# Optimization experiments

Measured on AMD Instinct MI355X. Metric: run time of the kernel, lower is better.

Reference implementation:

```python
import jax, jax.numpy as jnp
import numpy as np

_GELU = lambda x: jax.nn.gelu(x, approximate=False)  # torch nn.GELU default = exact erf


def setup_inputs():
    key = jax.random.key(0)
    ks = jax.random.split(key, 32)
    B, H = 16384, 768
    def p(i, shape):
        return jax.random.normal(ks[i], shape, jnp.float32) * 0.02
    return {
        "image_feat": jax.random.normal(ks[0], (B, H), jnp.float32),
        "text_feat": jax.random.normal(ks[1], (B, H), jnp.float32),
        "enhanced_image_feat": jax.random.normal(ks[2], (B, H), jnp.float32),
        "enhanced_text_feat": jax.random.normal(ks[3], (B, H), jnp.float32),
        "missing_type": jax.random.randint(ks[4], (B,), 0, 4),
        # info_encoder: H->256->64
        "info_w1": p(5, (H, 256)), "info_b1": jnp.zeros((256,), jnp.float32),
        "info_w2": p(6, (256, 64)), "info_b2": jnp.zeros((64,), jnp.float32),
        # modality_importance_predictor: H->H/2->1 (dropout inactive at eval)
        "imp_w1": p(7, (H, H // 2)), "imp_b1": jnp.zeros((H // 2,), jnp.float32),
        "imp_w2": p(8, (H // 2, 1)), "imp_b2": jnp.zeros((1,), jnp.float32),
        # feature_discriminator: H->256->64->1
        "disc_w1": p(9, (H, 256)), "disc_b1": jnp.zeros((256,), jnp.float32),
        "disc_w2": p(10, (256, 64)), "disc_b2": jnp.zeros((64,), jnp.float32),
        "disc_w3": p(11, (64, 1)), "disc_b3": jnp.zeros((1,), jnp.float32),
        # consistency_predictor: 2H->H->H/2->1
        "cons_w1": p(12, (2 * H, H)), "cons_b1": jnp.zeros((H,), jnp.float32),
        "cons_w2": p(13, (H, H // 2)), "cons_b2": jnp.zeros((H // 2,), jnp.float32),
        "cons_w3": p(14, (H // 2, 1)), "cons_b3": jnp.zeros((1,), jnp.float32),
        # task_difficulty_predictor: 2H->H->H/2->1
        "diff_w1": p(15, (2 * H, H)), "diff_b1": jnp.zeros((H,), jnp.float32),
        "diff_w2": p(16, (H, H // 2)), "diff_b2": jnp.zeros((H // 2,), jnp.float32),
        "diff_w3": p(17, (H // 2, 1)), "diff_b3": jnp.zeros((1,), jnp.float32),
    }


def _forward(image_feat, text_feat, enhanced_image_feat, enhanced_text_feat,
             info_w1, info_b1, info_w2, info_b2,
             imp_w1, imp_b1, imp_w2, imp_b2,
             disc_w1, disc_b1, disc_w2, disc_b2, disc_w3, disc_b3,
             cons_w1, cons_b1, cons_w2, cons_b2, cons_w3, cons_b3,
             diff_w1, diff_b1, diff_w2, diff_b2, diff_w3, diff_b3):
    sig = jax.nn.sigmoid

    def geometric(f):  # vectorized version of the per-sample python loop
        n = jnp.linalg.norm(f, axis=-1)
        nq = sig((n - 1.0) * 2.0)
        sp = jnp.mean((jnp.abs(f) > 0.01).astype(jnp.float32), axis=-1)
        sq = sig(jnp.std(f, axis=-1, ddof=1) * 10.0 - 1.0)  # torch.std is unbiased
        return (nq + sp + sq) / 3.0

    def information(f):
        enc = _GELU(f @ info_w1 + info_b1) @ info_w2 + info_b2  # [B,64]
        disc = jnp.round(sig(enc) * 10.0).astype(jnp.int32)     # values in 0..10
        # histogram-based entropy == the torch.unique loop (prob = count/64)
        counts = jnp.sum(disc[:, :, None] == jnp.arange(11, dtype=jnp.int32)[None, None, :], axis=1)
        prob = counts.astype(jnp.float32) / enc.shape[-1]
        ent = -jnp.sum(jnp.where(prob > 0, prob * jnp.log(prob + 1e-8), 0.0), axis=-1)
        eq = sig(ent - 2.0)
        # svd of a 1xD matrix has a single singular value = ||f||_2
        n = jnp.linalg.norm(f, axis=-1)
        cq = (n > 0.01).astype(jnp.float32) / f.shape[-1]
        fn = f / jnp.maximum(n, 1e-12)[:, None]  # F.normalize
        dq = sig(jnp.sum(fn * fn, axis=-1) - 0.5)
        return (eq + cq + dq) / 3.0

    def importance(f):
        return sig(_GELU(f @ imp_w1 + imp_b1) @ imp_w2 + imp_b2)[:, 0]

    def discrim(f):
        h = _GELU(f @ disc_w1 + disc_b1)
        h = _GELU(h @ disc_w2 + disc_b2)
        return sig(h @ disc_w3 + disc_b3)[:, 0]

    def head3(f, w1, b1, w2, b2, w3, b3):
        h = _GELU(f @ w1 + b1)
        h = _GELU(h @ w2 + b2)
        return sig(h @ w3 + b3)[:, 0]

    g_img = geometric(image_feat)
    g_txt = geometric(text_feat)
    g_eimg = geometric(enhanced_image_feat)
    g_etxt = geometric(enhanced_text_feat)
    i_img = information(image_feat)
    i_txt = information(text_feat)
    cons_o = head3(jnp.concatenate([image_feat, text_feat], -1), cons_w1, cons_b1, cons_w2, cons_b2, cons_w3, cons_b3)
    cons_e = head3(jnp.concatenate([enhanced_image_feat, enhanced_text_feat], -1), cons_w1, cons_b1, cons_w2, cons_b2, cons_w3, cons_b3)
    imp_i = importance(image_feat)
    imp_t = importance(text_feat)
    imp_ei = importance(enhanced_image_feat)
    imp_et = importance(enhanced_text_feat)
    auth_io = discrim(image_feat)
    auth_ie = discrim(enhanced_image_feat)
    auth_to = discrim(text_feat)
    auth_te = discrim(enhanced_text_feat)
    diff = head3(jnp.concatenate([enhanced_image_feat, enhanced_text_feat], -1), diff_w1, diff_b1, diff_w2, diff_b2, diff_w3, diff_b3)
    overall = (g_img + g_txt + i_img + i_txt + cons_e + (imp_i + imp_t) / 2.0) / 6.0
    return jnp.stack([g_img, g_txt, g_eimg, g_etxt, i_img, i_txt, cons_o, cons_e,
                      imp_i, imp_t, imp_ei, imp_et, auth_io, auth_ie, auth_to, auth_te,
                      diff, overall])  # [18, B]


def reference(image_feat, text_feat, enhanced_image_feat, enhanced_text_feat, missing_type,
              info_w1, info_b1, info_w2, info_b2,
              imp_w1, imp_b1, imp_w2, imp_b2,
              disc_w1, disc_b1, disc_w2, disc_b2, disc_w3, disc_b3,
              cons_w1, cons_b1, cons_w2, cons_b2, cons_w3, cons_b3,
              diff_w1, diff_b1, diff_w2, diff_b2, diff_w3, diff_b3):
    # missing_type is carried by the original forward but never used in the math
    return _forward(image_feat, text_feat, enhanced_image_feat, enhanced_text_feat,
                    info_w1, info_b1, info_w2, info_b2,
                    imp_w1, imp_b1, imp_w2, imp_b2,
                    disc_w1, disc_b1, disc_w2, disc_b2, disc_w3, disc_b3,
                    cons_w1, cons_b1, cons_w2, cons_b2, cons_w3, cons_b3,
                    diff_w1, diff_b1, diff_w2, diff_b2, diff_w3, diff_b3)
```

## Files before the change

### kernel.cpp

```cpp
#include <hip/hip_runtime.h>

typedef unsigned short bfu;
typedef __attribute__((ext_vector_type(8))) __bf16 bf16x8;
typedef __attribute__((ext_vector_type(4))) float f32x4;

__device__ __forceinline__ float bf2f(bfu u) {
    unsigned int x = ((unsigned int)u) << 16;
    return __builtin_bit_cast(float, x);
}
__device__ __forceinline__ bfu f2bf(float f) {
    unsigned int u = __builtin_bit_cast(unsigned int, f);
    unsigned int r = (u + 0x7fffu + ((u >> 16) & 1u)) >> 16;
    return (bfu)r;
}
__device__ __forceinline__ float sigm(float x) { return 1.0f / (1.0f + __expf(-x)); }
__device__ __forceinline__ float gelu_f(float x) {
    const float y = 0.7978845608f * (x + 0.044715f * x * x * x);
    const float t = 1.f - 2.f / (__expf(2.f * y) + 1.f);
    return 0.5f * x * (1.f + t);
}
__device__ __forceinline__ float gelu_x(float x) {
    return 0.5f * x * (1.0f + erff(x * 0.70710678118654752f));
}

__device__ __forceinline__ void async16(const void* g, void* l) {
    __builtin_amdgcn_global_load_lds((const __attribute__((address_space(1))) void*)g,
                                     (__attribute__((address_space(3))) void*)l, 16, 0, 0);
}

struct TDesc { const float* src; bfu* dst; int K, N, blk0; };
struct TPack { TDesc d[9]; };

__global__ __launch_bounds__(256) void transpose_k(TPack p) {
    const int bid = blockIdx.x;
    int j = 0;
#pragma unroll
    for (int i = 1; i < 9; ++i)
        if (bid >= p.d[i].blk0) j = i;
    const TDesc d = p.d[j];
    const int local = bid - d.blk0;
    const int tkn = d.K >> 6;
    const int tk = local % tkn, tn = local / tkn;
    const int k0 = tk * 64, n0 = tn * 64;
    __shared__ float tile[64][65];
    const int tx = threadIdx.x & 63, ty = threadIdx.x >> 6;
#pragma unroll
    for (int i = 0; i < 16; ++i) {
        const int r = ty * 16 + i;
        tile[r][tx] = d.src[(size_t)(k0 + r) * d.N + n0 + tx];
    }
    __syncthreads();
#pragma unroll
    for (int i = 0; i < 16; ++i) {
        const int n = ty * 16 + i;
        d.dst[(size_t)(n0 + n) * d.K + k0 + tx] = f2bf(tile[tx][n]);
    }
}

__global__ __launch_bounds__(256)
void prep_k(float* accz, int nacc, bfu* disc2pad, const float* w3,
            const float* b2, float* w3pad, float* b2pad) {
    const int i = blockIdx.x * 256 + threadIdx.x;
    if (i < nacc) accz[i] = 0.f;
    if (i < 64 * 256) disc2pad[64 * 256 + i] = 0;
    if (i < 128) {
        w3pad[i] = (i < 64) ? w3[i] : 0.f;
        b2pad[i] = (i < 64) ? b2[i] : 0.f;
    }
}

__global__ __launch_bounds__(256)
void geomcast_k(const float* F0, const float* F1, bfu* D0, bfu* D1,
                float* g0, float* g1, float* p0, float* p1) {
    const int z = blockIdx.y;
    const float* F = z ? F1 : F0;
    bfu* D = z ? D1 : D0;
    float* gout = z ? g1 : g0;
    float* part = z ? p1 : p0;
    const int wave = threadIdx.x >> 6, lane = threadIdx.x & 63;
    const int row = blockIdx.x * 4 + wave;
    const float* fr = F + (size_t)row * 768;
    bfu* dr = D + (size_t)row * 768;
    float sum = 0.f, ss = 0.f, cnt = 0.f;
#pragma unroll
    for (int i = 0; i < 3; ++i) {
        const float4 v = *(const float4*)(fr + i * 256 + lane * 4);
        sum += v.x + v.y + v.z + v.w;
        ss += v.x * v.x + v.y * v.y + v.z * v.z + v.w * v.w;
        cnt += ((fabsf(v.x) > 0.01f) ? 1.f : 0.f) + ((fabsf(v.y) > 0.01f) ? 1.f : 0.f) +
               ((fabsf(v.z) > 0.01f) ? 1.f : 0.f) + ((fabsf(v.w) > 0.01f) ? 1.f : 0.f);
        ushort4 b;
        b.x = f2bf(v.x); b.y = f2bf(v.y); b.z = f2bf(v.z); b.w = f2bf(v.w);
        *(ushort4*)(dr + i * 256 + lane * 4) = b;
    }
#pragma unroll
    for (int off = 32; off; off >>= 1) {
        sum += __shfl_xor(sum, off);
        ss  += __shfl_xor(ss, off);
        cnt += __shfl_xor(cnt, off);
    }
    if (lane == 0) {
        const float n = sqrtf(ss);
        const float nq = sigm((n - 1.f) * 2.f);
        const float sp = cnt * (1.f / 768.f);
        float var = (ss - sum * sum * (1.f / 768.f)) * (1.f / 767.f);
        var = fmaxf(var, 0.f);
        const float sq = sigm(sqrtf(var) * 10.f - 1.f);
        gout[row] = (nq + sp + sq) * (1.f / 3.f);
        if (part) {
            const float cq = (n > 0.01f) ? (1.f / 768.f) : 0.f;
            const float nc = fmaxf(n, 1e-12f);
            const float dq = sigm(ss / (nc * nc) - 0.5f);
            part[row] = (cq + dq) * (1.f / 3.f);
        }
    }
}

struct Seg {
    const bfu* A; const bfu* A2;
    const bfu* W;
    const float* bias;
    const float* dotw;
    bfu* C;
    float* acc;
    int ldc, mode, K, Ksplit, lda, Mtiles;
};
struct SegPack { Seg s[13]; };

__global__ __launch_bounds__(256)
void gemm_k(SegPack p) {
    constexpr int BK = 64, MT = 4, NT = 4;
    __shared__ bfu As0[128 * BK];
    __shared__ bfu Ws0[128 * BK];
    __shared__ bfu As1[128 * BK];
    __shared__ bfu Ws1[128 * BK];
    const int NTt = gridDim.x;
    const int g = blockIdx.y * NTt + blockIdx.x;
    const int G8 = NTt * 8;
    const int m = (g / G8) * 8 + (g & 7);
    const int n = (g % G8) >> 3;
    const Seg sg = p.s[n];
    if (m >= sg.Mtiles) return;
    const int t = threadIdx.x;
    const int wave = t >> 6, lane = t & 63;
    const int row_l = lane & 15, kq = lane >> 4;
    const int m0 = m * 128;
    const int wm = wave >> 1, wn = wave & 1;
    const int wrow0 = wm * 64, wcol0 = wn * 64;

    const int r0 = t >> 3;
    const int cc = ((t & 7) ^ (r0 & 7)) << 3;
    const size_t strA = (size_t)32 * sg.lda;
    const size_t strW = (size_t)32 * sg.K;
    const bfu* pA[4];
    const bfu* pW[4];
#pragma unroll
    for (int i = 0; i < 4; ++i) {
        pA[i] = sg.A + (size_t)(m0 + r0) * sg.lda + cc + i * strA;
        pW[i] = sg.W + (size_t)r0 * sg.K + cc + i * strW;
    }
    const int nkt = sg.K >> 6;
    const int ktsw = (sg.Ksplit < sg.K) ? (sg.Ksplit >> 6) : 0x7fffffff;

    f32x4 acc[MT][NT] = {};

    auto stage = [&](bfu* Ad, bfu* Wd, int sn) {
        if (sn == ktsw) {
#pragma unroll
            for (int i = 0; i < 4; ++i)
                pA[i] = sg.A2 + (size_t)(m0 + r0) * sg.lda + cc + i * strA;
        }
#pragma unroll
        for (int i = 0; i < 4; ++i)
            async16(pA[i], Ad + ((i * 256 + wave * 64) << 3));
#pragma unroll
        for (int i = 0; i < 4; ++i)
            async16(pW[i], Wd + ((i * 256 + wave * 64) << 3));
#pragma unroll
        for (int i = 0; i < 4; ++i) { pA[i] += BK; pW[i] += BK; }
    };
    auto compute = [&](const bfu* Ab, const bfu* Wb) {
#pragma unroll
        for (int ks = 0; ks < 2; ++ks) {
            bf16x8 af[MT], bfr[NT];
#pragma unroll
            for (int mi = 0; mi < MT; ++mi) {
                const int rA = wrow0 + mi * 16 + row_l;
                af[mi] = *(const bf16x8*)(Ab + rA * BK + (((ks * 4 + kq) ^ (rA & 7)) << 3));
            }
#pragma unroll
            for (int ni = 0; ni < NT; ++ni) {
                const int rB = wcol0 + ni * 16 + row_l;
                bfr[ni] = *(const bf16x8*)(Wb + rB * BK + (((ks * 4 + kq) ^ (rB & 7)) << 3));
            }
#pragma unroll
            for (int mi = 0; mi < MT; ++mi)
#pragma unroll
                for (int ni = 0; ni < NT; ++ni)
                    acc[mi][ni] = __builtin_amdgcn_mfma_f32_16x16x32_bf16(af[mi], bfr[ni], acc[mi][ni], 0, 0, 0);
        }
    };

    stage(As0, Ws0, 0);
    __syncthreads();
    for (int kt = 0; kt < nkt; kt += 2) {
        stage(As1, Ws1, kt + 1);
        compute(As0, Ws0);
        __syncthreads();
        if (kt + 2 < nkt) stage(As0, Ws0, kt + 2);
        compute(As1, Ws1);
        __syncthreads();
    }

    if (sg.mode == 0) {
#pragma unroll
        for (int ni = 0; ni < NT; ++ni) {
            const int col = wcol0 + ni * 16 + row_l;
            const float bv = sg.bias[col];
#pragma unroll
            for (int mi = 0; mi < MT; ++mi)
#pragma unroll
                for (int r = 0; r < 4; ++r) {
                    const int row = m0 + wrow0 + mi * 16 + kq * 4 + r;
                    sg.C[(size_t)row * sg.ldc + col] = f2bf(gelu_f(acc[mi][ni][r] + bv));
                }
        }
    } else if (sg.mode == 2) {
#pragma unroll
        for (int ni = 0; ni < NT; ++ni) {
            const int col = wcol0 + ni * 16 + row_l;
            const float bv = sg.bias[col];
#pragma unroll
            for (int mi = 0; mi < MT; ++mi)
#pragma unroll
                for (int r = 0; r < 4; ++r) {
                    const int row = m0 + wrow0 + mi * 16 + kq * 4 + r;
                    sg.C[(size_t)row * sg.ldc + col] = f2bf(gelu_x(acc[mi][ni][r] + bv));
                }
        }
    } else {
#pragma unroll
        for (int mi = 0; mi < MT; ++mi)
#pragma unroll
            for (int r = 0; r < 4; ++r) {
                float s = 0.f;
#pragma unroll
                for (int ni = 0; ni < NT; ++ni) {
                    const int col = wcol0 + ni * 16 + row_l;
                    s += sg.dotw[col] * gelu_f(acc[mi][ni][r] + sg.bias[col]);
                }
                s += __shfl_xor(s, 1); s += __shfl_xor(s, 2);
                s += __shfl_xor(s, 4); s += __shfl_xor(s, 8);
                if (row_l == 0)
                    atomicAdd(sg.acc + m0 + wrow0 + mi * 16 + kq * 4 + r, s);
            }
    }
}

__global__ __launch_bounds__(256)
void gemm64ent_k(const bfu* __restrict__ A, const bfu* __restrict__ W,
                 const float* __restrict__ bias, const float* __restrict__ part,
                 float* out, int B, int K, int lda) {
    constexpr int BK = 64, MT = 2, NT = 4;
    __shared__ __align__(16) float smemf[12288];
    bfu* As0 = (bfu*)smemf;
    bfu* Ws0 = (bfu*)smemf + 128 * BK;
    bfu* As1 = (bfu*)smemf + 192 * BK;
    bfu* Ws1 = (bfu*)smemf + 320 * BK;
    float* ET = smemf;
    const int t = threadIdx.x;
    const int wave = t >> 6, lane = t & 63;
    const int row_l = lane & 15, kq = lane >> 4;
    const int m0 = blockIdx.x * 128;
    const int wrow0 = wave * 32;
    f32x4 acc[MT][NT] = {};
    const int nkt = K / BK;

    const int r0 = t >> 3;
    const int cc = ((t & 7) ^ (r0 & 7)) << 3;
    const size_t strA = (size_t)32 * lda;
    const size_t strW = (size_t)32 * K;
    const bfu* pA[4];
    const bfu* pW[2];
#pragma unroll
    for (int i = 0; i < 4; ++i)
        pA[i] = A + (size_t)(m0 + r0) * lda + cc + i * strA;
#pragma unroll
    for (int i = 0; i < 2; ++i)
        pW[i] = W + (size_t)r0 * K + cc + i * strW;

    auto stage = [&](bfu* Ad, bfu* Wd) {
#pragma unroll
        for (int i = 0; i < 4; ++i)
            async16(pA[i], Ad + ((i * 256 + wave * 64) << 3));
#pragma unroll
        for (int i = 0; i < 2; ++i)
            async16(pW[i], Wd + ((i * 256 + wave * 64) << 3));
#pragma unroll
        for (int i = 0; i < 4; ++i) pA[i] += BK;
#pragma unroll
        for (int i = 0; i < 2; ++i) pW[i] += BK;
    };
    auto compute = [&](const bfu* Ab, const bfu* Wb) {
#pragma unroll
        for (int ks = 0; ks < 2; ++ks) {
            bf16x8 af[MT], bfr[NT];
#pragma unroll
            for (int mi = 0; mi < MT; ++mi) {
                const int rA = wrow0 + mi * 16 + row_l;
                af[mi] = *(const bf16x8*)(Ab + rA * BK + (((ks * 4 + kq) ^ (rA & 7)) << 3));
            }
#pragma unroll
            for (int ni = 0; ni < NT; ++ni) {
                const int rB = ni * 16 + row_l;
                bfr[ni] = *(const bf16x8*)(Wb + rB * BK + (((ks * 4 + kq) ^ (rB & 7)) << 3));
            }
#pragma unroll
            for (int mi = 0; mi < MT; ++mi)
#pragma unroll
                for (int ni = 0; ni < NT; ++ni)
                    acc[mi][ni] = __builtin_amdgcn_mfma_f32_16x16x32_bf16(af[mi], bfr[ni], acc[mi][ni], 0, 0, 0);
        }
    };

    stage(As0, Ws0);
    __syncthreads();
    for (int kt = 0; kt < nkt; kt += 2) {
        stage(As1, Ws1);
        compute(As0, Ws0);
        __syncthreads();
        if (kt + 2 < nkt) stage(As0, Ws0);
        compute(As1, Ws1);
        __syncthreads();
    }

#pragma unroll
    for (int mi = 0; mi < MT; ++mi)
#pragma unroll
        for (int ni = 0; ni < NT; ++ni) {
            const int col = ni * 16 + row_l;
            const float bv = bias[col];
#pragma unroll
            for (int r = 0; r < 4; ++r)
                ET[(wrow0 + mi * 16 + kq * 4 + r) * 65 + col] = acc[mi][ni][r] + bv;
        }
    __syncthreads();
    if (t < 128) {
        int cnt[11];
#pragma unroll
        for (int b = 0; b < 11; ++b) cnt[b] = 0;
        for (int j = 0; j < 64; ++j) {
            const int d = (int)rintf(sigm(ET[t * 65 + j]) * 10.f);
#pragma unroll
            for (int b = 0; b < 11; ++b) cnt[b] += (d == b);
        }
        float ent = 0.f;
#pragma unroll
        for (int b = 0; b < 11; ++b) {
            if (cnt[b] > 0) {
                const float pp = (float)cnt[b] * (1.f / 64.f);
                ent -= pp * __logf(pp + 1e-8f);
            }
        }
        const int row = m0 + t;
        const int orow = (row < B) ? 4 : 5;
        const int rl = (row < B) ? row : row - B;
        out[(size_t)orow * B + rl] = part[row] + sigm(ent - 2.f) * (1.f / 3.f);
    }
}

__global__ __launch_bounds__(256)
void finalize_k(float* out, const float* a_imp1, const float* a_imp2,
                const float* a_co, const float* a_ce, const float* a_df,
                const float* a_d1, const float* a_d2,
                const float* imp_b2, const float* disc_b3,
                const float* cons_b3, const float* diff_b3, int B) {
    const int i = blockIdx.x * 256 + threadIdx.x;
    if (i >= B) return;
    const float ib = imp_b2[0], db = disc_b3[0], cb = cons_b3[0], fb = diff_b3[0];
    const float o6 = sigm(a_co[i] + cb);
    const float o7 = sigm(a_ce[i] + cb);
    const float o8 = sigm(a_imp1[i] + ib);
    const float o9 = sigm(a_imp1[B + i] + ib);
    out[6 * B + i] = o6;
    out[7 * B + i] = o7;
    out[8 * B + i] = o8;
    out[9 * B + i] = o9;
    out[10 * B + i] = sigm(a_imp2[i] + ib);
    out[11 * B + i] = sigm(a_imp2[B + i] + ib);
    out[12 * B + i] = sigm(a_d1[i] + db);
    out[14 * B + i] = sigm(a_d1[B + i] + db);
    out[13 * B + i] = sigm(a_d2[i] + db);
    out[15 * B + i] = sigm(a_d2[B + i] + db);
    out[16 * B + i] = sigm(a_df[i] + fb);
    const float v = out[0 * B + i] + out[1 * B + i] + out[4 * B + i] + out[5 * B + i] +
                    o7 + 0.5f * (o8 + o9);
    out[17 * B + i] = v * (1.f / 6.f);
}

extern "C" void kernel_launch(void* const* d_in, const int* in_sizes, int n_in,
                              void* d_out, int out_size, void* d_ws, size_t ws_size,
                              hipStream_t stream) {
    const int B = in_sizes[4];
    const int B2 = 2 * B;
    float* out = (float*)d_out;
    const float* img  = (const float*)d_in[0];
    const float* txt  = (const float*)d_in[1];
    const float* eimg = (const float*)d_in[2];
    const float* etxt = (const float*)d_in[3];
    const float* info_w1 = (const float*)d_in[5];  const float* info_b1 = (const float*)d_in[6];
    const float* info_w2 = (const float*)d_in[7];  const float* info_b2 = (const float*)d_in[8];
    const float* imp_w1  = (const float*)d_in[9];  const float* imp_b1  = (const float*)d_in[10];
    const float* imp_w2  = (const float*)d_in[11]; const float* imp_b2  = (const float*)d_in[12];
    const float* disc_w1 = (const float*)d_in[13]; const float* disc_b1 = (const float*)d_in[14];
    const float* disc_w2 = (const float*)d_in[15]; const float* disc_b2 = (const float*)d_in[16];
    const float* disc_w3 = (const float*)d_in[17]; const float* disc_b3 = (const float*)d_in[18];
    const float* cons_w1 = (const float*)d_in[19]; const float* cons_b1 = (const float*)d_in[20];
    const float* cons_w2 = (const float*)d_in[21]; const float* cons_b2 = (const float*)d_in[22];
    const float* cons_w3 = (const float*)d_in[23]; const float* cons_b3 = (const float*)d_in[24];
    const float* diff_w1 = (const float*)d_in[25]; const float* diff_b1 = (const float*)d_in[26];
    const float* diff_w2 = (const float*)d_in[27]; const float* diff_b2 = (const float*)d_in[28];
    const float* diff_w3 = (const float*)d_in[29]; const float* diff_b3 = (const float*)d_in[30];

    char* wsp = (char*)d_ws;
    size_t off = 0;
    auto alloc = [&](size_t bytes) -> void* {
        void* p = wsp + off;
        off += (bytes + 255) & ~(size_t)255;
        return p;
    };
    bfu* info1t = (bfu*)alloc((size_t)256 * 768 * 2);
    bfu* info2t = (bfu*)alloc((size_t)64 * 256 * 2);
    bfu* imp1t  = (bfu*)alloc((size_t)384 * 768 * 2);
    bfu* disc1t = (bfu*)alloc((size_t)256 * 768 * 2);
    bfu* disc2p = (bfu*)alloc((size_t)128 * 256 * 2);
    bfu* cons1t = (bfu*)alloc((size_t)768 * 1536 * 2);
    bfu* cons2t = (bfu*)alloc((size_t)384 * 768 * 2);
    bfu* diff1t = (bfu*)alloc((size_t)768 * 1536 * 2);
    bfu* diff2t = (bfu*)alloc((size_t)384 * 768 * 2);
    float* w3pad = (float*)alloc(128 * 4);
    float* b2pad = (float*)alloc(128 * 4);
    float* part = (float*)alloc((size_t)B2 * 4);
    float* accz = (float*)alloc((size_t)11 * B * 4);
    float* a_imp1 = accz;
    float* a_imp2 = accz + B2;
    float* a_co = accz + 2 * B2;
    float* a_ce = a_co + B;
    float* a_df = a_ce + B;
    float* a_d1 = a_df + B;
    float* a_d2 = a_d1 + B2;
    bfu* fA01 = (bfu*)alloc((size_t)B2 * 768 * 2);
    bfu* X    = (bfu*)alloc((size_t)B * 2048 * 2);
    bfu* Hd   = X;
    bfu* Hi   = X + (size_t)B * 512;
    bfu* Hc_c = X + (size_t)B * 512;
    bfu* Hc_d = X + (size_t)B * 1280;
    (void)ws_size; (void)n_in; (void)out_size;

    prep_k<<<dim3((11 * B + 255) / 256), 256, 0, stream>>>(accz, 11 * B, disc2p,
                                                           disc_w3, disc_b2, w3pad, b2pad);
    TPack tp;
    int blk = 0, ti = 0;
    auto setd = [&](const float* s, bfu* d, int K, int N) {
        tp.d[ti++] = {s, d, K, N, blk};
        blk += (K / 64) * (N / 64);
    };
    setd(info_w1, info1t, 768, 256);
    setd(info_w2, info2t, 256, 64);
    setd(imp_w1, imp1t, 768, 384);
    setd(disc_w1, disc1t, 768, 256);
    setd(disc_w2, disc2p, 256, 64);
    setd(cons_w1, cons1t, 1536, 768);
    setd(cons_w2, cons2t, 768, 384);
    setd(diff_w1, diff1t, 1536, 768);
    setd(diff_w2, diff2t, 768, 384);
    transpose_k<<<dim3(blk), 256, 0, stream>>>(tp);

    auto st_seg = [&](const bfu* A, const bfu* A2, const bfu* W, const float* b,
                      bfu* C, int ldc, int mode, int K, int Ksplit, int lda, int Mt) -> Seg {
        return Seg{A, A2, W, b, nullptr, C, nullptr, ldc, mode, K, Ksplit, lda, Mt};
    };
    auto dt_seg = [&](const bfu* A, const bfu* W, const float* b, const float* dw,
                      float* acc, int K, int lda, int Mt) -> Seg {
        return Seg{A, nullptr, W, b, dw, nullptr, acc, 0, 1, K, K, lda, Mt};
    };
    const bfu* fB = fA01 + (size_t)B * 768;
    const int MT2 = B2 / 128, MT1 = B / 128;

    geomcast_k<<<dim3(B / 4, 2), 256, 0, stream>>>(img, txt, fA01, (bfu*)fB,
                                                   out + 0 * B, out + 1 * B, part, part + B);
    {
        SegPack p;
        p.s[0] = st_seg(fA01, nullptr, info1t, info_b1, Hi, 256, 2, 768, 768, 768, MT2);
        p.s[1] = st_seg(fA01, nullptr, info1t + (size_t)128 * 768, info_b1 + 128, Hi + 128, 256, 2, 768, 768, 768, MT2);
        for (int i = 0; i < 3; ++i)
            p.s[2 + i] = dt_seg(fA01, imp1t + (size_t)128 * i * 768, imp_b1 + 128 * i,
                                imp_w2 + 128 * i, a_imp1, 768, 768, MT2);
        p.s[5] = st_seg(fA01, nullptr, disc1t, disc_b1, Hd, 256, 0, 768, 768, 768, MT2);
        p.s[6] = st_seg(fA01, nullptr, disc1t + (size_t)128 * 768, disc_b1 + 128, Hd + 128, 256, 0, 768, 768, 768, MT2);
        gemm_k<<<dim3(7, MT2), 256, 0, stream>>>(p);
    }
    gemm64ent_k<<<dim3(MT2), 256, 0, stream>>>(Hi, info2t, info_b2, part, out, B, 256, 256);
    {
        SegPack p;
        p.s[0] = dt_seg(Hd, disc2p, b2pad, w3pad, a_d1, 256, 256, MT2);
        for (int i = 0; i < 6; ++i)
            p.s[1 + i] = st_seg(fA01, fB, cons1t + (size_t)128 * i * 1536,
                                cons_b1 + 128 * i, Hc_c + 128 * i, 768, 0, 1536, 768, 768, MT1);
        gemm_k<<<dim3(7, MT2), 256, 0, stream>>>(p);
    }

    geomcast_k<<<dim3(B / 4, 2), 256, 0, stream>>>(eimg, etxt, fA01, (bfu*)fB,
                                                   out + 2 * B, out + 3 * B, nullptr, nullptr);
    {
        SegPack p;
        for (int i = 0; i < 3; ++i)
            p.s[i] = dt_seg(fA01, imp1t + (size_t)128 * i * 768, imp_b1 + 128 * i,
                            imp_w2 + 128 * i, a_imp2, 768, 768, MT2);
        p.s[3] = st_seg(fA01, nullptr, disc1t, disc_b1, Hd, 256, 0, 768, 768, 768, MT2);
        p.s[4] = st_seg(fA01, nullptr, disc1t + (size_t)128 * 768, disc_b1 + 128, Hd + 128, 256, 0, 768, 768, 768, MT2);
        for (int i = 0; i < 3; ++i)
            p.s[5 + i] = dt_seg(Hc_c, cons2t + (size_t)128 * i * 768, cons_b2 + 128 * i,
                                cons_w3 + 128 * i, a_co, 768, 768, MT1);
        gemm_k<<<dim3(8, MT2), 256, 0, stream>>>(p);
    }
    {
        SegPack p;
        p.s[0] = dt_seg(Hd, disc2p, b2pad, w3pad, a_d2, 256, 256, MT2);
        for (int i = 0; i < 6; ++i) {
            p.s[1 + i] = st_seg(fA01, fB, cons1t + (size_t)128 * i * 1536,
                                cons_b1 + 128 * i, Hc_c + 128 * i, 768, 0, 1536, 768, 768, MT1);
            p.s[7 + i] = st_seg(fA01, fB, diff1t + (size_t)128 * i * 1536,
                                diff_b1 + 128 * i, Hc_d + 128 * i, 768, 0, 1536, 768, 768, MT1);
        }
        gemm_k<<<dim3(13, MT2), 256, 0, stream>>>(p);
    }
    {
        SegPack p;
        for (int i = 0; i < 3; ++i) {
            p.s[i]     = dt_seg(Hc_c, cons2t + (size_t)128 * i * 768, cons_b2 + 128 * i,
                                cons_w3 + 128 * i, a_ce, 768, 768, MT1);
            p.s[3 + i] = dt_seg(Hc_d, diff2t + (size_t)128 * i * 768, diff_b2 + 128 * i,
                                diff_w3 + 128 * i, a_df, 768, 768, MT1);
        }
        gemm_k<<<dim3(6, MT1), 256, 0, stream>>>(p);
    }

    finalize_k<<<dim3((B + 255) / 256), 256, 0, stream>>>(out, a_imp1, a_imp2, a_co, a_ce,
                                                          a_df, a_d1, a_d2,
                                                          imp_b2, disc_b3, cons_b3, diff_b3, B);
}
```

Measured before the change: 690.8 us.

## Deepen GEMM prefetch with counted vmcnt waits instead of full syncthreads

Both GEMM kernels now issue loads for two K-tiles before the loop. Each compute step waits only on the older tile's loads, using s_waitcnt vmcnt with a fixed count plus a raw s_barrier, instead of a full __syncthreads that drains all outstanding memory operations. The next tile is staged right after each compute, so global loads stay in flight across compute phases. The hardcoded vmcnt counts must match the number of loads issued per stage call; if they do not, the code can race.

```diff
diff --git a/kernel.cpp b/kernel.cpp
--- a/kernel.cpp
+++ b/kernel.cpp
@@ -202,14 +202,23 @@
     };
 
     stage(As0, Ws0, 0);
-    __syncthreads();
+    stage(As1, Ws1, 1);
     for (int kt = 0; kt < nkt; kt += 2) {
-        stage(As1, Ws1, kt + 1);
+        asm volatile("s_waitcnt vmcnt(8)" ::: "memory");
+        __builtin_amdgcn_s_barrier();
+        __builtin_amdgcn_sched_barrier(0);
         compute(As0, Ws0);
-        __syncthreads();
+        __builtin_amdgcn_sched_barrier(0);
+        __builtin_amdgcn_s_barrier();
         if (kt + 2 < nkt) stage(As0, Ws0, kt + 2);
+        if (kt + 2 < nkt) { asm volatile("s_waitcnt vmcnt(8)" ::: "memory"); }
+        else              { asm volatile("s_waitcnt vmcnt(0)" ::: "memory"); }
+        __builtin_amdgcn_s_barrier();
+        __builtin_amdgcn_sched_barrier(0);
         compute(As1, Ws1);
-        __syncthreads();
+        __builtin_amdgcn_sched_barrier(0);
+        __builtin_amdgcn_s_barrier();
+        if (kt + 3 < nkt) stage(As1, Ws1, kt + 3);
     }
 
     if (sg.mode == 0) {
@@ -324,14 +333,23 @@
     };
 
     stage(As0, Ws0);
-    __syncthreads();
+    stage(As1, Ws1);
     for (int kt = 0; kt < nkt; kt += 2) {
-        stage(As1, Ws1);
+        asm volatile("s_waitcnt vmcnt(6)" ::: "memory");
+        __builtin_amdgcn_s_barrier();
+        __builtin_amdgcn_sched_barrier(0);
         compute(As0, Ws0);
-        __syncthreads();
+        __builtin_amdgcn_sched_barrier(0);
+        __builtin_amdgcn_s_barrier();
         if (kt + 2 < nkt) stage(As0, Ws0);
+        if (kt + 2 < nkt) { asm volatile("s_waitcnt vmcnt(6)" ::: "memory"); }
+        else              { asm volatile("s_waitcnt vmcnt(0)" ::: "memory"); }
+        __builtin_amdgcn_s_barrier();
+        __builtin_amdgcn_sched_barrier(0);
         compute(As1, Ws1);
-        __syncthreads();
+        __builtin_amdgcn_sched_barrier(0);
+        __builtin_amdgcn_s_barrier();
+        if (kt + 3 < nkt) stage(As1, Ws1);
     }
 
 #pragma unroll
```

Result: no change. 689.4 us (-0.2%).

## Merge setup kernels and regroup GEMM launches to cut launch count and tails

Applied to the files above, without the earlier changes.

Folds the weight transposes, accumulator zeroing and the casts of all four feature tensors into one setup kernel. A separate bf16 buffer for the enhanced features lets the original-feature cons layer-1 GEMM run together with the first-stage info/imp/disc GEMM. The disc layer-2 GEMM and the info-entropy GEMM now share one launch, and the entropy binning loop is split across all 256 threads. This removes several launches and low-occupancy tail kernels, at the cost of extra workspace and a larger, more heterogeneous setup grid.

```diff
diff --git a/kernel.cpp b/kernel.cpp
--- a/kernel.cpp
+++ b/kernel.cpp
@@ -30,42 +30,91 @@
 
 struct TDesc { const float* src; bfu* dst; int K, N, blk0; };
 struct TPack { TDesc d[9]; };
-
-__global__ __launch_bounds__(256) void transpose_k(TPack p) {
+struct GeoArgs { const float* F; bfu* D; float* gout; float* part; };
+struct SetupPack {
+    TPack tp; int nT, nP, Bq;
+    float* accz; int nacc; bfu* disc2pad;
+    const float* w3f; const float* b2f; float* w3pad; float* b2pad;
+    GeoArgs g[4]; int ng;
+};
+
+__global__ __launch_bounds__(256) void setup_k(SetupPack s) {
+    __shared__ float tile[64][65];
     const int bid = blockIdx.x;
-    int j = 0;
-#pragma unroll
-    for (int i = 1; i < 9; ++i)
-        if (bid >= p.d[i].blk0) j = i;
-    const TDesc d = p.d[j];
-    const int local = bid - d.blk0;
-    const int tkn = d.K >> 6;
-    const int tk = local % tkn, tn = local / tkn;
-    const int k0 = tk * 64, n0 = tn * 64;
-    __shared__ float tile[64][65];
-    const int tx = threadIdx.x & 63, ty = threadIdx.x >> 6;
-#pragma unroll
-    for (int i = 0; i < 16; ++i) {
-        const int r = ty * 16 + i;
-        tile[r][tx] = d.src[(size_t)(k0 + r) * d.N + n0 + tx];
-    }
-    __syncthreads();
-#pragma unroll
-    for (int i = 0; i < 16; ++i) {
-        const int n = ty * 16 + i;
-        d.dst[(size_t)(n0 + n) * d.K + k0 + tx] = f2bf(tile[tx][n]);
-    }
-}
-
-__global__ __launch_bounds__(256)
-void prep_k(float* accz, int nacc, bfu* disc2pad, const float* w3,
-            const float* b2, float* w3pad, float* b2pad) {
-    const int i = blockIdx.x * 256 + threadIdx.x;
-    if (i < nacc) accz[i] = 0.f;
-    if (i < 64 * 256) disc2pad[64 * 256 + i] = 0;
-    if (i < 128) {
-        w3pad[i] = (i < 64) ? w3[i] : 0.f;
-        b2pad[i] = (i < 64) ? b2[i] : 0.f;
+    if (bid < s.nT) {
+        int j = 0;
+#pragma unroll
+        for (int i = 1; i < 9; ++i)
+            if (bid >= s.tp.d[i].blk0) j = i;
+        const TDesc d = s.tp.d[j];
+        const int local = bid - d.blk0;
+        const int tkn = d.K >> 6;
+        const int tk = local % tkn, tn = local / tkn;
+        const int k0 = tk * 64, n0 = tn * 64;
+        const int tx = threadIdx.x & 63, ty = threadIdx.x >> 6;
+#pragma unroll
+        for (int i = 0; i < 16; ++i) {
+            const int r = ty * 16 + i;
+            tile[r][tx] = d.src[(size_t)(k0 + r) * d.N + n0 + tx];
+        }
+        __syncthreads();
+#pragma unroll
+        for (int i = 0; i < 16; ++i) {
+            const int n = ty * 16 + i;
+            d.dst[(size_t)(n0 + n) * d.K + k0 + tx] = f2bf(tile[tx][n]);
+        }
+        return;
+    }
+    int b2 = bid - s.nT;
+    if (b2 < s.nP) {
+        const int i = b2 * 256 + threadIdx.x;
+        if (i < s.nacc) s.accz[i] = 0.f;
+        if (i < 64 * 256) s.disc2pad[64 * 256 + i] = 0;
+        if (i < 128) {
+            s.w3pad[i] = (i < 64) ? s.w3f[i] : 0.f;
+            s.b2pad[i] = (i < 64) ? s.b2f[i] : 0.f;
+        }
+        return;
+    }
+    b2 -= s.nP;
+    const int gi = b2 / s.Bq, rb = b2 % s.Bq;
+    const GeoArgs ga = s.g[gi];
+    const int wave = threadIdx.x >> 6, lane = threadIdx.x & 63;
+    const int row = rb * 4 + wave;
+    const float* fr = ga.F + (size_t)row * 768;
+    bfu* dr = ga.D + (size_t)row * 768;
+    float sum = 0.f, ss = 0.f, cnt = 0.f;
+#pragma unroll
+    for (int i = 0; i < 3; ++i) {
+        const float4 v = *(const float4*)(fr + i * 256 + lane * 4);
+        sum += v.x + v.y + v.z + v.w;
+        ss += v.x * v.x + v.y * v.y + v.z * v.z + v.w * v.w;
+        cnt += ((fabsf(v.x) > 0.01f) ? 1.f : 0.f) + ((fabsf(v.y) > 0.01f) ? 1.f : 0.f) +
+               ((fabsf(v.z) > 0.01f) ? 1.f : 0.f) + ((fabsf(v.w) > 0.01f) ? 1.f : 0.f);
+        ushort4 b;
+        b.x = f2bf(v.x); b.y = f2bf(v.y); b.z = f2bf(v.z); b.w = f2bf(v.w);
+        *(ushort4*)(dr + i * 256 + lane * 4) = b;
+    }
+#pragma unroll
+    for (int off = 32; off; off >>= 1) {
+        sum += __shfl_xor(sum, off);
+        ss  += __shfl_xor(ss, off);
+        cnt += __shfl_xor(cnt, off);
+    }
+    if (lane == 0) {
+        const float n = sqrtf(ss);
+        const float nq = sigm((n - 1.f) * 2.f);
+        const float sp = cnt * (1.f / 768.f);
+        float var = (ss - sum * sum * (1.f / 768.f)) * (1.f / 767.f);
+        var = fmaxf(var, 0.f);
+        const float sq = sigm(sqrtf(var) * 10.f - 1.f);
+        ga.gout[row] = (nq + sp + sq) * (1.f / 3.f);
+        if (ga.part) {
+            const float cq = (n > 0.01f) ? (1.f / 768.f) : 0.f;
+            const float nc = fmaxf(n, 1e-12f);
+            const float dq = sigm(ss / (nc * nc) - 0.5f);
+            ga.part[row] = (cq + dq) * (1.f / 3.f);
+        }
     }
 }
 
@@ -127,15 +176,13 @@
 };
 struct SegPack { Seg s[13]; };
 
-__global__ __launch_bounds__(256)
-void gemm_k(SegPack p) {
+__device__ __forceinline__ void gemm_body(const SegPack& p, int bx, int by, int NTt, bfu* LDSb) {
     constexpr int BK = 64, MT = 4, NT = 4;
-    __shared__ bfu As0[128 * BK];
-    __shared__ bfu Ws0[128 * BK];
-    __shared__ bfu As1[128 * BK];
-    __shared__ bfu Ws1[128 * BK];
-    const int NTt = gridDim.x;
-    const int g = blockIdx.y * NTt + blockIdx.x;
+    bfu* As0 = LDSb;
+    bfu* Ws0 = LDSb + 8192;
+    bfu* As1 = LDSb + 16384;
+    bfu* Ws1 = LDSb + 24576;
+    const int g = by * NTt + bx;
     const int G8 = NTt * 8;
     const int m = (g / G8) * 8 + (g & 7);
     const int n = (g % G8) >> 3;
@@ -258,20 +305,33 @@
 }
 
 __global__ __launch_bounds__(256)
-void gemm64ent_k(const bfu* __restrict__ A, const bfu* __restrict__ W,
-                 const float* __restrict__ bias, const float* __restrict__ part,
-                 float* out, int B, int K, int lda) {
+void gemm_k(SegPack p) {
+    __shared__ bfu LDS[32768];
+    gemm_body(p, blockIdx.x, blockIdx.y, gridDim.x, LDS);
+}
+
+__global__ __launch_bounds__(256)
+void big2ent_k(SegPack p, const bfu* __restrict__ A, const bfu* __restrict__ W,
+               const float* __restrict__ bias, const float* __restrict__ part,
+               float* out, int B) {
+    __shared__ __align__(16) char smemc[65536];
+    if (blockIdx.x == 0) {
+        gemm_body(p, 0, blockIdx.y, 1, (bfu*)smemc);
+        return;
+    }
     constexpr int BK = 64, MT = 2, NT = 4;
-    __shared__ __align__(16) float smemf[12288];
+    float* smemf = (float*)smemc;
     bfu* As0 = (bfu*)smemf;
-    bfu* Ws0 = (bfu*)smemf + 128 * BK;
-    bfu* As1 = (bfu*)smemf + 192 * BK;
-    bfu* Ws1 = (bfu*)smemf + 320 * BK;
+    bfu* Ws0 = (bfu*)smemf + 8192;
+    bfu* As1 = (bfu*)smemf + 12288;
+    bfu* Ws1 = (bfu*)smemf + 20480;
     float* ET = smemf;
+    int* CN = (int*)(smemc + 33280);
+    const int K = 256, lda = 256;
     const int t = threadIdx.x;
     const int wave = t >> 6, lane = t & 63;
     const int row_l = lane & 15, kq = lane >> 4;
-    const int m0 = blockIdx.x * 128;
+    const int m0 = blockIdx.y * 128;
     const int wrow0 = wave * 32;
     f32x4 acc[MT][NT] = {};
     const int nkt = K / BK;
@@ -345,20 +405,27 @@
                 ET[(wrow0 + mi * 16 + kq * 4 + r) * 65 + col] = acc[mi][ni][r] + bv;
         }
     __syncthreads();
+    {
+        const int row = t & 127, hf = t >> 7;
+        int cnt[11];
+#pragma unroll
+        for (int b = 0; b < 11; ++b) cnt[b] = 0;
+        for (int j = hf * 32; j < hf * 32 + 32; ++j) {
+            const int d = (int)rintf(sigm(ET[row * 65 + j]) * 10.f);
+#pragma unroll
+            for (int b = 0; b < 11; ++b) cnt[b] += (d == b);
+        }
+#pragma unroll
+        for (int b = 0; b < 11; ++b) CN[t * 11 + b] = cnt[b];
+    }
+    __syncthreads();
     if (t < 128) {
-        int cnt[11];
-#pragma unroll
-        for (int b = 0; b < 11; ++b) cnt[b] = 0;
-        for (int j = 0; j < 64; ++j) {
-            const int d = (int)rintf(sigm(ET[t * 65 + j]) * 10.f);
-#pragma unroll
-            for (int b = 0; b < 11; ++b) cnt[b] += (d == b);
-        }
         float ent = 0.f;
 #pragma unroll
         for (int b = 0; b < 11; ++b) {
-            if (cnt[b] > 0) {
-                const float pp = (float)cnt[b] * (1.f / 64.f);
+            const int c = CN[t * 11 + b] + CN[(t + 128) * 11 + b];
+            if (c > 0) {
+                const float pp = (float)c * (1.f / 64.f);
                 ent -= pp * __logf(pp + 1e-8f);
             }
         }
@@ -453,16 +520,21 @@
     bfu* X    = (bfu*)alloc((size_t)B * 2048 * 2);
     bfu* Hd   = X;
     bfu* Hi   = X + (size_t)B * 512;
-    bfu* Hc_c = X + (size_t)B * 512;
-    bfu* Hc_d = X + (size_t)B * 1280;
-    (void)ws_size; (void)n_in; (void)out_size;
-
-    prep_k<<<dim3((11 * B + 255) / 256), 256, 0, stream>>>(accz, 11 * B, disc2p,
-                                                           disc_w3, disc_b2, w3pad, b2pad);
-    TPack tp;
+    bfu* HcA  = X + (size_t)B * 1024;
+    bfu* HcB  = X + (size_t)B * 512;
+    bfu* HcC  = X + (size_t)B * 1280;
+    const size_t fA2_bytes = (size_t)B2 * 768 * 2;
+    bfu* fA2 = (bfu*)(wsp + off);
+    const bool bigws = (off + fA2_bytes) <= ws_size;
+    if (bigws) off += (fA2_bytes + 255) & ~(size_t)255;
+    const bfu* fph2  = bigws ? fA2 : fA01;
+    const bfu* fph2B = fph2 + (size_t)B * 768;
+    (void)n_in; (void)out_size;
+
+    SetupPack sp{};
     int blk = 0, ti = 0;
     auto setd = [&](const float* s, bfu* d, int K, int N) {
-        tp.d[ti++] = {s, d, K, N, blk};
+        sp.tp.d[ti++] = {s, d, K, N, blk};
         blk += (K / 64) * (N / 64);
     };
     setd(info_w1, info1t, 768, 256);
@@ -474,7 +546,17 @@
     setd(cons_w2, cons2t, 768, 384);
     setd(diff_w1, diff1t, 1536, 768);
     setd(diff_w2, diff2t, 768, 384);
-    transpose_k<<<dim3(blk), 256, 0, stream>>>(tp);
+    sp.nT = blk;
+    sp.nP = (11 * B + 255) / 256;
+    sp.Bq = B / 4;
+    sp.accz = accz; sp.nacc = 11 * B; sp.disc2pad = disc2p;
+    sp.w3f = disc_w3; sp.b2f = disc_b2; sp.w3pad = w3pad; sp.b2pad = b2pad;
+    sp.g[0] = {img, fA01, out + 0 * B, part};
+    sp.g[1] = {txt, fA01 + (size_t)B * 768, out + 1 * B, part + B};
+    sp.g[2] = {eimg, fA2, out + 2 * B, nullptr};
+    sp.g[3] = {etxt, fA2 + (size_t)B * 768, out + 3 * B, nullptr};
+    sp.ng = bigws ? 4 : 2;
+    setup_k<<<dim3(sp.nT + sp.nP + sp.ng * sp.Bq), 256, 0, stream>>>(sp);
 
     auto st_seg = [&](const bfu* A, const bfu* A2, const bfu* W, const float* b,
                       bfu* C, int ldc, int mode, int K, int Ksplit, int lda, int Mt) -> Seg {
@@ -487,10 +569,8 @@
     const bfu* fB = fA01 + (size_t)B * 768;
     const int MT2 = B2 / 128, MT1 = B / 128;
 
-    geomcast_k<<<dim3(B / 4, 2), 256, 0, stream>>>(img, txt, fA01, (bfu*)fB,
-                                                   out + 0 * B, out + 1 * B, part, part + B);
     {
-        SegPack p;
+        SegPack p{};
         p.s[0] = st_seg(fA01, nullptr, info1t, info_b1, Hi, 256, 2, 768, 768, 768, MT2);
         p.s[1] = st_seg(fA01, nullptr, info1t + (size_t)128 * 768, info_b1 + 128, Hi + 128, 256, 2, 768, 768, 768, MT2);
         for (int i = 0; i < 3; ++i)
@@ -498,49 +578,51 @@
                                 imp_w2 + 128 * i, a_imp1, 768, 768, MT2);
         p.s[5] = st_seg(fA01, nullptr, disc1t, disc_b1, Hd, 256, 0, 768, 768, 768, MT2);
         p.s[6] = st_seg(fA01, nullptr, disc1t + (size_t)128 * 768, disc_b1 + 128, Hd + 128, 256, 0, 768, 768, 768, MT2);
-        gemm_k<<<dim3(7, MT2), 256, 0, stream>>>(p);
-    }
-    gemm64ent_k<<<dim3(MT2), 256, 0, stream>>>(Hi, info2t, info_b2, part, out, B, 256, 256);
+        for (int i = 0; i < 6; ++i)
+            p.s[7 + i] = st_seg(fA01, fB, cons1t + (size_t)128 * i * 1536,
+                                cons_b1 + 128 * i, HcA + 128 * i, 768, 0, 1536, 768, 768, MT1);
+        gemm_k<<<dim3(13, MT2), 256, 0, stream>>>(p);
+    }
+
     {
-        SegPack p;
+        SegPack p{};
         p.s[0] = dt_seg(Hd, disc2p, b2pad, w3pad, a_d1, 256, 256, MT2);
-        for (int i = 0; i < 6; ++i)
-            p.s[1 + i] = st_seg(fA01, fB, cons1t + (size_t)128 * i * 1536,
-                                cons_b1 + 128 * i, Hc_c + 128 * i, 768, 0, 1536, 768, 768, MT1);
-        gemm_k<<<dim3(7, MT2), 256, 0, stream>>>(p);
-    }
-
-    geomcast_k<<<dim3(B / 4, 2), 256, 0, stream>>>(eimg, etxt, fA01, (bfu*)fB,
-                                                   out + 2 * B, out + 3 * B, nullptr, nullptr);
+        big2ent_k<<<dim3(2, MT2), 256, 0, stream>>>(p, Hi, info2t, info_b2, part, out, B);
+    }
+
+    if (!bigws)
+        geomcast_k<<<dim3(B / 4, 2), 256, 0, stream>>>(eimg, etxt, fA01, (bfu*)fB,
+                                                       out + 2 * B, out + 3 * B, nullptr, nullptr);
+
     {
-        SegPack p;
+        SegPack p{};
         for (int i = 0; i < 3; ++i)
-            p.s[i] = dt_seg(fA01, imp1t + (size_t)128 * i * 768, imp_b1 + 128 * i,
+            p.s[i] = dt_seg(fph2, imp1t + (size_t)128 * i * 768, imp_b1 + 128 * i,
                             imp_w2 + 128 * i, a_imp2, 768, 768, MT2);
-        p.s[3] = st_seg(fA01, nullptr, disc1t, disc_b1, Hd, 256, 0, 768, 768, 768, MT2);
-        p.s[4] = st_seg(fA01, nullptr, disc1t + (size_t)128 * 768, disc_b1 + 128, Hd + 128, 256, 0, 768, 768, 768, MT2);
+        p.s[3] = st_seg(fph2, nullptr, disc1t, disc_b1, Hd, 256, 0, 768, 768, 768, MT2);
+        p.s[4] = st_seg(fph2, nullptr, disc1t + (size_t)128 * 768, disc_b1 + 128, Hd + 128, 256, 0, 768, 768, 768, MT2);
         for (int i = 0; i < 3; ++i)
-            p.s[5 + i] = dt_seg(Hc_c, cons2t + (size_t)128 * i * 768, cons_b2 + 128 * i,
+            p.s[5 + i] = dt_seg(HcA, cons2t + (size_t)128 * i * 768, cons_b2 + 128 * i,
                                 cons_w3 + 128 * i, a_co, 768, 768, MT1);
         gemm_k<<<dim3(8, MT2), 256, 0, stream>>>(p);
     }
     {
-        SegPack p;
+        SegPack p{};
         p.s[0] = dt_seg(Hd, disc2p, b2pad, w3pad, a_d2, 256, 256, MT2);
         for (int i = 0; i < 6; ++i) {
-            p.s[1 + i] = st_seg(fA01, fB, cons1t + (size_t)128 * i * 1536,
-                                cons_b1 + 128 * i, Hc_c + 128 * i, 768, 0, 1536, 768, 768, MT1);
-            p.s[7 + i] = st_seg(fA01, fB, diff1t + (size_t)128 * i * 1536,
-                                diff_b1 + 128 * i, Hc_d + 128 * i, 768, 0, 1536, 768, 768, MT1);
+            p.s[1 + i] = st_seg(fph2, fph2B, cons1t + (size_t)128 * i * 1536,
+                                cons_b1 + 128 * i, HcB + 128 * i, 768, 0, 1536, 768, 768, MT1);
+            p.s[7 + i] = st_seg(fph2, fph2B, diff1t + (size_t)128 * i * 1536,
+                                diff_b1 + 128 * i, HcC + 128 * i, 768, 0, 1536, 768, 768, MT1);
         }
         gemm_k<<<dim3(13, MT2), 256, 0, stream>>>(p);
     }
     {
-        SegPack p;
+        SegPack p{};
         for (int i = 0; i < 3; ++i) {
-            p.s[i]     = dt_seg(Hc_c, cons2t + (size_t)128 * i * 768, cons_b2 + 128 * i,
+            p.s[i]     = dt_seg(HcB, cons2t + (size_t)128 * i * 768, cons_b2 + 128 * i,
                                 cons_w3 + 128 * i, a_ce, 768, 768, MT1);
-            p.s[3 + i] = dt_seg(Hc_d, diff2t + (size_t)128 * i * 768, diff_b2 + 128 * i,
+            p.s[3 + i] = dt_seg(HcC, diff2t + (size_t)128 * i * 768, diff_b2 + 128 * i,
                                 diff_w3 + 128 * i, a_df, 768, 768, MT1);
         }
         gemm_k<<<dim3(6, MT1), 256, 0, stream>>>(p);
```

Result: faster. 675.9 us (-2.1%).
